# Kernel tuning notes

Measured on AMD Instinct MI355X. Metric: run time of the kernel, lower is better.

## Reference

```python
import jax, jax.numpy as jnp
import numpy as np

B, V, T = 64, 196, 64       # batch, visual tokens, text tokens
VIS, TXT, E = 768, 768, 512  # backbone dims, joint embed dim


def l2norm(x):
    return x / jnp.maximum(jnp.linalg.norm(x, axis=-1, keepdims=True), 1e-12)


def setup_inputs() -> dict:
    key = jax.random.key(0)
    ks = jax.random.split(key, 16)
    f = lambda k, s: jax.random.normal(k, s, dtype=jnp.float32)
    return {
        'v_cls': f(ks[0], (B, VIS)),
        'v_tok': f(ks[1], (B, V, VIS)),
        't_cls': f(ks[2], (B, TXT)),
        't_tok': f(ks[3], (B, T, TXT)),
        'Wv_cls': f(ks[4], (VIS, E)) * 0.02, 'bv_cls': jnp.zeros((E,), jnp.float32),
        'Wt_cls': f(ks[5], (TXT, E)) * 0.02, 'bt_cls': jnp.zeros((E,), jnp.float32),
        'Wv_tok': f(ks[6], (VIS, E)) * 0.02, 'bv_tok': jnp.zeros((E,), jnp.float32),
        'Wt_tok': f(ks[7], (TXT, E)) * 0.02, 'bt_tok': jnp.zeros((E,), jnp.float32),
        'wv_fc': f(ks[8], (E,)) * 0.02, 'bv_fc': jnp.zeros((), jnp.float32),
        'wt_fc': f(ks[9], (E,)) * 0.02, 'bt_fc': jnp.zeros((), jnp.float32),
        'text_length': jax.random.randint(ks[10], (B,), 16, T + 1),
    }


def reference(v_cls, v_tok, t_cls, t_tok,
              Wv_cls, bv_cls, Wt_cls, bt_cls,
              Wv_tok, bv_tok, Wt_tok, bt_tok,
              wv_fc, bv_fc, wt_fc, bt_fc, text_length):
    ve_cls = v_cls @ Wv_cls + bv_cls
    te_cls = t_cls @ Wt_cls + bt_cls
    ve = v_tok @ Wv_tok + bv_tok          # [B, V, E]
    te = t_tok @ Wt_tok + bt_tok          # [B, T, E]

    # per-token scalar weights (Linear(E, 1).squeeze(2))
    vw = ve @ wv_fc + bv_fc               # [B, V]
    tw = te @ wt_fc + bt_fc               # [B, T]

    # mask padded text positions (pos >= length), then softmax
    pad = jnp.arange(T)[None, :] >= text_length[:, None]
    tw = jax.nn.softmax(jnp.where(pad, -jnp.inf, tw), axis=-1)
    vw = jax.nn.softmax(vw, axis=-1)

    ve = l2norm(ve)
    te = l2norm(te)

    # full cross-batch token similarity [b, q, v, t]
    sim = jnp.einsum('bvd,qtd->bqvt', ve, te)
    image_to_text = jnp.einsum('bqv,bv->bq', sim.max(axis=-1), vw)
    text_to_image = jnp.einsum('bqt,qt->bq', sim.max(axis=2), tw)

    # diagonal (b == q) similarities drive the cdcr gathers
    sim_diag = jnp.einsum('bvd,btd->bvt', ve, te)
    idx1 = jnp.argmax(sim_diag, axis=-1)   # [B, V] best text token per visual token
    idx2 = jnp.argmax(sim_diag, axis=1)    # [B, T] best visual token per text token
    max_v = jnp.take_along_axis(ve, idx2[:, :, None], axis=1).reshape(-1, E)  # [B*T, E]
    max_t = jnp.take_along_axis(te, idx1[:, :, None], axis=1).reshape(-1, E)  # [B*V, E]

    t_feat = te.reshape(-1, E)
    v_feat = ve.reshape(-1, E)

    def zn(x):  # torch .std() is unbiased (ddof=1)
        return (x - x.mean(axis=0)) / jnp.std(x, axis=0, ddof=1)

    c1 = jnp.einsum('ac,ad,a->cd', zn(t_feat), zn(max_v), tw.reshape(-1)) / B
    c2 = jnp.einsum('ac,ad,a->cd', zn(v_feat), zn(max_t), vw.reshape(-1)) / B
    c = (c1 + c2) / 2.0

    D = c.shape[0]
    on_diag = jnp.sum((jnp.diagonal(c) - 1.0) ** 2)
    off_diag = jnp.sum(c.reshape(-1)[1:].reshape(D - 1, D + 1)[:, :-1] ** 2)
    cdcr_loss = 0.1 * (on_diag * 1.0 + off_diag * 0.06)

    return image_to_text, text_to_image, cdcr_loss
```

## Files before the change

kernel.cpp:

```cpp
#include <hip/hip_runtime.h>
#include <cstddef>

#define EDIM 512
#define KDIM 768
#define NB 64
#define NV 196
#define NT 64
#define MROWS_V (NB * NV)
#define MROWS_T (NB * NT)

typedef __attribute__((ext_vector_type(8))) short bf16x8;
typedef __attribute__((ext_vector_type(4))) float f32x4;

static __device__ inline unsigned short f2bf(float f) {
  unsigned u = __float_as_uint(f);
  unsigned r = (u + 0x7fff + ((u >> 16) & 1)) >> 16;
  return (unsigned short)r;
}
static __device__ inline float bf2f(short s) {
  return __uint_as_float(((unsigned)(unsigned short)s) << 16);
}
static __device__ __forceinline__ int swz4(int r) { return (r + (r >> 2)) & 3; }

static __device__ __forceinline__ void gload16(const void* g, void* l) {
  __builtin_amdgcn_global_load_lds(
      (const __attribute__((address_space(1))) void*)g,
      (__attribute__((address_space(3))) void*)l, 16, 0, 0);
}

__global__ void k_prep(const float* __restrict__ va, short* __restrict__ vo, int na8,
                       const float* __restrict__ ta, short* __restrict__ to, int nb8,
                       const float* __restrict__ W0, const float* __restrict__ W1,
                       short* __restrict__ T0, short* __restrict__ T1) {
  __shared__ float tile[32][33];
  int blk = blockIdx.x;
  int tid = threadIdx.x;
  if (blk < 6240) {
    int i = blk * 256 + tid;
    const float* in; short* outp; int idx;
    if (i < na8) { in = va; outp = vo; idx = i; }
    else { idx = i - na8; if (idx >= nb8) return; in = ta; outp = to; }
    float4 a = *(const float4*)(in + (size_t)idx * 8);
    float4 b = *(const float4*)(in + (size_t)idx * 8 + 4);
    bf16x8 v;
    v[0] = (short)f2bf(a.x); v[1] = (short)f2bf(a.y);
    v[2] = (short)f2bf(a.z); v[3] = (short)f2bf(a.w);
    v[4] = (short)f2bf(b.x); v[5] = (short)f2bf(b.y);
    v[6] = (short)f2bf(b.z); v[7] = (short)f2bf(b.w);
    *(bf16x8*)(outp + (size_t)idx * 8) = v;
  } else {
    int z = blk - 6240;
    int bx = z % 24, by = (z / 24) % 16, bz = z / 384;
    const float* W = bz ? W1 : W0;
    short*       T = bz ? T1 : T0;
    int k0 = bx * 32, n0 = by * 32;
    int tx = tid & 31, ty = tid >> 5;
    for (int i = ty; i < 32; i += 8)
      tile[i][tx] = W[(size_t)(k0 + i) * EDIM + n0 + tx];
    __syncthreads();
    for (int i = ty; i < 32; i += 8)
      T[(size_t)(n0 + i) * KDIM + k0 + tx] = (short)f2bf(tile[tx][i]);
  }
}

__global__ __launch_bounds__(256, 4) void k_proj_mfma2(
    const short* __restrict__ vX, const short* __restrict__ tX,
    const short* __restrict__ WvT, const short* __restrict__ WtT,
    const float* __restrict__ vb, const float* __restrict__ tb,
    short* __restrict__ vout, short* __restrict__ tout) {
  __shared__ short As[2][128 * 32];
  __shared__ short Bs[2][128 * 32];
  int y = blockIdx.y;
  const short* Xbf; const short* WT; const float* bias; short* Mbf; int r0;
  if (y < 98) { Xbf = vX; WT = WvT; bias = vb; Mbf = vout; r0 = y * 128; }
  else        { Xbf = tX; WT = WtT; bias = tb; Mbf = tout; r0 = (y - 98) * 128; }
  int n0 = blockIdx.x * 128;
  int tid = threadIdx.x;
  int w = tid >> 6, lane = tid & 63, lg = lane >> 4, li = lane & 15;
  int fsw = (li + (li >> 2)) & 3;

  const short* aSrc[2];
  const short* bSrc[2];
#pragma unroll
  for (int uu = 0; uu < 2; ++uu) {
    int u = uu * 256 + w * 64 + lane;
    int row = u >> 2, seg = u & 3;
    int ss = seg ^ swz4(row);
    aSrc[uu] = Xbf + (size_t)(r0 + row) * KDIM + ss * 8;
    bSrc[uu] = WT + (size_t)(n0 + row) * KDIM + ss * 8;
  }

  auto stage = [&](int bb) {
    short* Ad = &As[bb][0];
    short* Bd = &Bs[bb][0];
#pragma unroll
    for (int uu = 0; uu < 2; ++uu) {
      gload16(aSrc[uu], Ad + (uu * 256 + w * 64) * 8);
      aSrc[uu] += 32;
      gload16(bSrc[uu], Bd + (uu * 256 + w * 64) * 8);
      bSrc[uu] += 32;
    }
  };

  f32x4 acc[2][8];
#pragma unroll
  for (int i = 0; i < 2; ++i)
#pragma unroll
    for (int j = 0; j < 8; ++j) acc[i][j] = (f32x4){0.f, 0.f, 0.f, 0.f};

  stage(0);
  int cur = 0;
  const int NKC = KDIM / 32;
  for (int kc = 0; kc < NKC; ++kc) {
    __builtin_amdgcn_s_barrier();
    if (kc < NKC - 1) {
      stage(cur ^ 1);
      asm volatile("s_waitcnt vmcnt(4)" ::: "memory");
    } else {
      asm volatile("s_waitcnt vmcnt(0)" ::: "memory");
    }
    __builtin_amdgcn_s_barrier();
    const short* Ab = &As[cur][0];
    const short* Bb = &Bs[cur][0];
    bf16x8 bfr[8];
#pragma unroll
    for (int j = 0; j < 8; ++j)
      bfr[j] = *(const bf16x8*)(Bb + (j * 16 + li) * 32 + (lg ^ fsw) * 8);
    __builtin_amdgcn_s_setprio(1);
#pragma unroll
    for (int i = 0; i < 2; ++i) {
      bf16x8 afr = *(const bf16x8*)(Ab + ((w * 2 + i) * 16 + li) * 32 + (lg ^ fsw) * 8);
#pragma unroll
      for (int j = 0; j < 8; ++j)
        acc[i][j] = __builtin_amdgcn_mfma_f32_16x16x32_bf16(afr, bfr[j], acc[i][j], 0, 0, 0);
    }
    __builtin_amdgcn_s_setprio(0);
    cur ^= 1;
  }
#pragma unroll
  for (int j = 0; j < 8; ++j) {
    int n = n0 + j * 16 + li;
    float bb = bias[n];
#pragma unroll
    for (int i = 0; i < 2; ++i)
#pragma unroll
      for (int reg = 0; reg < 4; ++reg)
        Mbf[(size_t)(r0 + (w * 2 + i) * 16 + lg * 4 + reg) * EDIM + n] =
            (short)f2bf(acc[i][j][reg] + bb);
  }
}

__global__ void k_normfc2(short* __restrict__ vM, short* __restrict__ tM,
                          const float* __restrict__ vfcw, const float* __restrict__ tfcw,
                          const float* __restrict__ vfcb, const float* __restrict__ tfcb,
                          float* __restrict__ vwout, float* __restrict__ twout) {
  int blk = blockIdx.x;
  short* Mbf; const float* fcw; const float* fcb; float* wout; int row;
  if (blk < 3136) { Mbf = vM; fcw = vfcw; fcb = vfcb; wout = vwout;
                    row = blk * 4 + (threadIdx.x >> 6); if (row >= 12544) return; }
  else            { Mbf = tM; fcw = tfcw; fcb = tfcb; wout = twout;
                    row = (blk - 3136) * 4 + (threadIdx.x >> 6); if (row >= 4096) return; }
  int lane = threadIdx.x & 63;
  short* p = Mbf + (size_t)row * EDIM + lane * 8;
  bf16x8 v = *(bf16x8*)p;
  float4 w0 = *(const float4*)(fcw + lane * 8);
  float4 w1 = *(const float4*)(fcw + lane * 8 + 4);
  float a[8];
#pragma unroll
  for (int j = 0; j < 8; ++j) a[j] = bf2f(v[j]);
  float dot = a[0] * w0.x + a[1] * w0.y + a[2] * w0.z + a[3] * w0.w +
              a[4] * w1.x + a[5] * w1.y + a[6] * w1.z + a[7] * w1.w;
  float ss = a[0] * a[0] + a[1] * a[1] + a[2] * a[2] + a[3] * a[3] +
             a[4] * a[4] + a[5] * a[5] + a[6] * a[6] + a[7] * a[7];
  for (int s = 1; s < 64; s <<= 1) {
    dot += __shfl_xor(dot, s);
    ss += __shfl_xor(ss, s);
  }
  float inv = 1.0f / fmaxf(sqrtf(ss), 1e-12f);
#pragma unroll
  for (int j = 0; j < 8; ++j) v[j] = (short)f2bf(a[j] * inv);
  *(bf16x8*)p = v;
  if (lane == 0) wout[row] = dot + fcb[0];
}

__global__ void k_softmax(float* __restrict__ vwf, float* __restrict__ twf,
                          const int* __restrict__ tlen) {
  __shared__ float red[8];
  int tid = threadIdx.x;
  if (blockIdx.x < 64) {
    int b = blockIdx.x;
    float x = (tid < NV) ? vwf[b * NV + tid] : -1e30f;
    float m = x;
    for (int s = 1; s < 64; s <<= 1) m = fmaxf(m, __shfl_xor(m, s));
    if ((tid & 63) == 0) red[tid >> 6] = m;
    __syncthreads();
    m = fmaxf(fmaxf(red[0], red[1]), fmaxf(red[2], red[3]));
    float e = (tid < NV) ? expf(x - m) : 0.0f;
    float s = e;
    for (int st = 1; st < 64; st <<= 1) s += __shfl_xor(s, st);
    if ((tid & 63) == 0) red[4 + (tid >> 6)] = s;
    __syncthreads();
    s = red[4] + red[5] + red[6] + red[7];
    if (tid < NV) vwf[b * NV + tid] = e / s;
  } else {
    int b = blockIdx.x - 64;
    if (tid < 64) {
      int len = tlen[b];
      float x = twf[b * NT + tid];
      bool valid = tid < len;
      float xv = valid ? x : -1e30f;
      float m = xv;
      for (int s = 1; s < 64; s <<= 1) m = fmaxf(m, __shfl_xor(m, s));
      float e = valid ? expf(x - m) : 0.0f;
      float s = e;
      for (int st = 1; st < 64; st <<= 1) s += __shfl_xor(s, st);
      twf[b * NT + tid] = e / s;
    }
  }
}

__global__ __launch_bounds__(512, 4) void k_sim(
    const short* __restrict__ ve_bf, const short* __restrict__ te_bf,
    const float* __restrict__ vwf, const float* __restrict__ twf,
    float* __restrict__ out, int* __restrict__ gMT, int* __restrict__ gMV) {
  __shared__ short As[2][208 * 32];
  __shared__ short Bs[2][128 * 32];
  __shared__ float colv[8][64];
  __shared__ int   coli[8][64];
  __shared__ float redp[8];
  int n = blockIdx.x;
  int xcd = n & 7, idx = n >> 3;
  int b = xcd * 8 + (idx & 7);
  int qq = idx >> 3;
  int tid = threadIdx.x;
  int w = tid >> 6, lane = tid & 63, lg = lane >> 4, li = lane & 15;
  int qsel = w >> 2, wr = w & 3;
  int q = 2 * qq + qsel;
  const short* Abf = ve_bf + (size_t)b * NV * EDIM;
  const short* Bbf = te_bf + (size_t)qq * 128 * EDIM;
  int fsw = (li + (li >> 2)) & 3;
  int nt = wr ? 3 : 4;
  int tbase = wr ? (1 + wr * 3) : 0;

  const short* aSrc[2];
#pragma unroll
  for (int uu = 0; uu < 2; ++uu) {
    int u = uu * 512 + w * 64 + lane;
    int row = u >> 2;
    if (row > NV - 1) row = NV - 1;
    int seg = u & 3;
    int ss = seg ^ swz4(row);
    aSrc[uu] = Abf + (size_t)row * EDIM + ss * 8;
  }
  const short* bSrc;
  {
    int u = tid;
    int row = u >> 2, seg = u & 3;
    int ss = seg ^ swz4(row);
    bSrc = Bbf + (size_t)row * EDIM + ss * 8;
  }

  auto stage = [&](int bb) {
    short* Ad = &As[bb][0];
    short* Bd = &Bs[bb][0];
    gload16(bSrc, Bd + (w * 64) * 8);
    bSrc += 32;
#pragma unroll
    for (int uu = 0; uu < 2; ++uu) {
      int u0 = uu * 512 + w * 64;
      if (u0 < NV * 4) {
        gload16(aSrc[uu], Ad + u0 * 8);
        aSrc[uu] += 32;
      }
    }
  };

  f32x4 acc[4][4];
#pragma unroll
  for (int i = 0; i < 4; ++i)
#pragma unroll
    for (int j = 0; j < 4; ++j) acc[i][j] = (f32x4){0.f, 0.f, 0.f, 0.f};

  stage(0);
  int cur = 0;
  for (int kc = 0; kc < 16; ++kc) {
    __builtin_amdgcn_s_barrier();
    if (kc < 15) {
      stage(cur ^ 1);
      if (w <= 4) asm volatile("s_waitcnt vmcnt(3)" ::: "memory");
      else        asm volatile("s_waitcnt vmcnt(2)" ::: "memory");
    } else {
      asm volatile("s_waitcnt vmcnt(0)" ::: "memory");
    }
    __builtin_amdgcn_s_barrier();
    const short* Ab2 = &As[cur][0];
    const short* Bb2 = &Bs[cur][0];
    bf16x8 bfr[4];
#pragma unroll
    for (int j = 0; j < 4; ++j)
      bfr[j] = *(const bf16x8*)(Bb2 + (qsel * 64 + j * 16 + li) * 32 + (lg ^ fsw) * 8);
    __builtin_amdgcn_s_setprio(1);
#pragma unroll
    for (int i = 0; i < 4; ++i) {
      if (i < nt) {
        bf16x8 afr = *(const bf16x8*)(Ab2 + ((tbase + i) * 16 + li) * 32 + (lg ^ fsw) * 8);
#pragma unroll
        for (int j = 0; j < 4; ++j)
          acc[i][j] = __builtin_amdgcn_mfma_f32_16x16x32_bf16(afr, bfr[j], acc[i][j], 0, 0, 0);
      }
    }
    __builtin_amdgcn_s_setprio(0);
    cur ^= 1;
  }

  bool diag = (b == q);
  bool diagblk = (b >> 1) == qq;
  float ip = 0.f;

  if (diagblk) {
#pragma unroll
    for (int i = 0; i < 4; ++i) {
      if (i < nt) {
#pragma unroll
        for (int reg = 0; reg < 4; ++reg) {
          int v = (tbase + i) * 16 + lg * 4 + reg;
          float m = acc[i][0][reg];
          int ti = li;
#pragma unroll
          for (int j = 1; j < 4; ++j) {
            float vv = acc[i][j][reg];
            int t = j * 16 + li;
            if (vv > m) { m = vv; ti = t; }
          }
          for (int d = 1; d < 16; d <<= 1) {
            float om = __shfl_xor(m, d);
            int oi = __shfl_xor(ti, d);
            if (om > m || (om == m && oi < ti)) { m = om; ti = oi; }
          }
          if (li == 0 && v < NV) {
            ip += vwf[b * NV + v] * m;
            if (diag) gMT[b * NV + v] = b * NT + ti;
          }
        }
      }
    }
    float cm[4]; int cv[4];
#pragma unroll
    for (int j = 0; j < 4; ++j) { cm[j] = -3.0e38f; cv[j] = 0; }
#pragma unroll
    for (int i = 0; i < 4; ++i) {
      if (i < nt) {
#pragma unroll
        for (int reg = 0; reg < 4; ++reg) {
          int v = (tbase + i) * 16 + lg * 4 + reg;
          bool ok = v < NV;
#pragma unroll
          for (int j = 0; j < 4; ++j) {
            float s = ok ? acc[i][j][reg] : -3.0e38f;
            if (s > cm[j]) { cm[j] = s; cv[j] = v; }
          }
        }
      }
    }
#pragma unroll
    for (int j = 0; j < 4; ++j) {
      for (int d = 16; d < 64; d <<= 1) {
        float om = __shfl_xor(cm[j], d);
        int ov = __shfl_xor(cv[j], d);
        if (om > cm[j] || (om == cm[j] && ov < cv[j])) { cm[j] = om; cv[j] = ov; }
      }
      if (lg == 0) { colv[w][j * 16 + li] = cm[j]; coli[w][j * 16 + li] = cv[j]; }
    }
  } else {
#pragma unroll
    for (int i = 0; i < 4; ++i) {
      if (i < nt) {
#pragma unroll
        for (int reg = 0; reg < 4; ++reg) {
          int v = (tbase + i) * 16 + lg * 4 + reg;
          float m = fmaxf(fmaxf(acc[i][0][reg], acc[i][1][reg]),
                          fmaxf(acc[i][2][reg], acc[i][3][reg]));
          for (int d = 1; d < 16; d <<= 1) m = fmaxf(m, __shfl_xor(m, d));
          if (li == 0 && v < NV) ip += vwf[b * NV + v] * m;
        }
      }
    }
    float cm[4];
#pragma unroll
    for (int j = 0; j < 4; ++j) cm[j] = -3.0e38f;
#pragma unroll
    for (int i = 0; i < 4; ++i) {
      if (i < nt) {
#pragma unroll
      for (int reg = 0; reg < 4; ++reg) {
          int v = (tbase + i) * 16 + lg * 4 + reg;
          bool ok = v < NV;
#pragma unroll
          for (int j = 0; j < 4; ++j)
            cm[j] = fmaxf(cm[j], ok ? acc[i][j][reg] : -3.0e38f);
        }
      }
    }
#pragma unroll
    for (int j = 0; j < 4; ++j) {
      for (int d = 16; d < 64; d <<= 1) cm[j] = fmaxf(cm[j], __shfl_xor(cm[j], d));
      if (lg == 0) colv[w][j * 16 + li] = cm[j];
    }
  }
  for (int d = 1; d < 64; d <<= 1) ip += __shfl_xor(ip, d);
  if (lane == 0) redp[w] = ip;
  __syncthreads();
  if (tid < 128) {
    int qs = tid >> 6, t = tid & 63;
    int qe = 2 * qq + qs;
    float m = colv[qs * 4][t];
    if (diagblk) {
      int bi = coli[qs * 4][t];
#pragma unroll
      for (int w2 = 1; w2 < 4; ++w2) {
        float om = colv[qs * 4 + w2][t];
        int ov = coli[qs * 4 + w2][t];
        if (om > m || (om == m && ov < bi)) { m = om; bi = ov; }
      }
      if (b == qe) gMV[b * NT + t] = b * NV + bi;
    } else {
#pragma unroll
      for (int w2 = 1; w2 < 4; ++w2) m = fmaxf(m, colv[qs * 4 + w2][t]);
    }
    float p = twf[qe * NT + t] * m;
    for (int d = 1; d < 64; d <<= 1) p += __shfl_xor(p, d);
    if ((tid & 63) == 0) out[4096 + b * 64 + qe] = p;
  }
  if (tid == 0) {
    out[b * 64 + 2 * qq]     = redp[0] + redp[1] + redp[2] + redp[3];
    out[b * 64 + 2 * qq + 1] = redp[4] + redp[5] + redp[6] + redp[7];
  }
}

__global__ void k_materialize(const short* __restrict__ ve_bf, const short* __restrict__ te_bf,
                              const int* __restrict__ gMT, const int* __restrict__ gMV,
                              const float* __restrict__ vwf, const float* __restrict__ twf,
                              short* __restrict__ tTw, short* __restrict__ mvT,
                              short* __restrict__ vTw, short* __restrict__ mtT,
                              float* __restrict__ statPart) {
  int z = blockIdx.z;
  int at = blockIdx.x, ct = blockIdx.y;
  int K = (z == 2 || z == 3) ? MROWS_V : MROWS_T;
  if (at * 64 >= K) return;
  const short* src; const int* g = 0; short* dst;
  bool applyW;
  const float* wS = (z <= 1) ? twf : vwf;
  if (z == 0)      { src = te_bf; dst = tTw; applyW = true;  }
  else if (z == 1) { src = ve_bf; g = gMV; dst = mvT; applyW = false; }
  else if (z == 2) { src = ve_bf; dst = vTw; applyW = true;  }
  else             { src = te_bf; g = gMT; dst = mtT; applyW = false; }
  __shared__ float tile[64][67];
  __shared__ float wrow[64];
  int tid = threadIdx.x;
  for (int u = tid; u < 512; u += 256) {
    int a = u >> 3, cseg = (u & 7) << 3;
    int ga = at * 64 + a;
    int row = g ? g[ga] : ga;
    bf16x8 vv = *(const bf16x8*)(src + (size_t)row * EDIM + ct * 64 + cseg);
#pragma unroll
    for (int j = 0; j < 8; j++) tile[a][cseg + j] = bf2f(vv[j]);
    if ((u & 7) == 0) wrow[a] = wS[ga];
  }
  __syncthreads();
  for (int u = tid; u < 512; u += 256) {
    int c = u >> 3, aseg = (u & 7) << 3;
    bf16x8 ov;
#pragma unroll
    for (int j = 0; j < 8; j++) {
      float x = tile[aseg + j][c];
      if (applyW) x *= wrow[aseg + j];
      ov[j] = (short)f2bf(x);
    }
    int kchunk = at * 2 + (aseg >> 5);
    *(bf16x8*)(dst + ((size_t)kchunk * 512 + ct * 64 + c) * 32 + (aseg & 31)) = ov;
  }
  int cl = tid >> 2, part = tid & 3;
  float s = 0, ssq = 0, sw = 0;
  for (int a = part * 16; a < part * 16 + 16; ++a) {
    float x = tile[a][cl];
    s += x; ssq += x * x; sw += wrow[a] * x;
  }
  for (int d = 1; d < 4; d <<= 1) {
    s += __shfl_xor(s, d); ssq += __shfl_xor(ssq, d); sw += __shfl_xor(sw, d);
  }
  if (part == 0) {
    int cbase = (z == 0) ? 0 : (z == 1) ? 64 : (z == 2) ? 128 : 324;
    size_t sidx = ((size_t)(cbase + at) * 512 + ct * 64 + cl) * 3;
    statPart[sidx] = s; statPart[sidx + 1] = ssq; statPart[sidx + 2] = sw;
  }
}

__global__ void k_statfin(const float* __restrict__ statPart, float* __restrict__ stats) {
  int m = blockIdx.x, c = threadIdx.x;
  int R = (m < 2) ? MROWS_T : MROWS_V;
  int nchunk = (m < 2) ? 64 : 196;
  int base = (m == 0) ? 0 : (m == 1) ? 64 : (m == 2) ? 128 : 324;
  float s = 0, ss = 0, sw = 0;
  for (int ch = 0; ch < nchunk; ch++) {
    size_t idx = ((size_t)(base + ch) * 512 + c) * 3;
    s += statPart[idx]; ss += statPart[idx + 1]; sw += statPart[idx + 2];
  }
  float mean = s / R;
  float var = (ss - s * mean) / (R - 1);
  float rstd = 1.0f / sqrtf(var);
  stats[(m * 3 + 0) * 512 + c] = mean;
  stats[(m * 3 + 1) * 512 + c] = rstd;
  stats[(m * 3 + 2) * 512 + c] = sw;
}

__global__ __launch_bounds__(512, 2) void k_wgemm2(
    const short* __restrict__ tTw, const short* __restrict__ mvT,
    const short* __restrict__ vTw, const short* __restrict__ mtT,
    float* __restrict__ Spart) {
  __shared__ short As[2][128 * 32];
  __shared__ short Bs[2][128 * 32];
  int c0 = blockIdx.x * 128, d0 = blockIdx.y * 128;
  int z = blockIdx.z;
  int which = z >> 3, slice = z & 7;
  const short* A = which ? vTw : tTw;
  const short* B = which ? mtT : mvT;
  int K = which ? MROWS_V : MROWS_T;
  int nch = (K >> 3) >> 5;
  size_t a0c = (size_t)slice * nch;
  int tid = threadIdx.x;
  int w = tid >> 6, lane = tid & 63, lg = lane >> 4, li = lane & 15;
  int fsw = (li + (li >> 2)) & 3;

  const short* aSrc; const short* bSrc;
  {
    int row = tid >> 2, seg = tid & 3;
    int ss = seg ^ swz4(row);
    aSrc = A + (a0c * 512 + (size_t)(c0 + row)) * 32 + ss * 8;
    bSrc = B + (a0c * 512 + (size_t)(d0 + row)) * 32 + ss * 8;
  }

  auto stage = [&](int bb) {
    gload16(aSrc, &As[bb][0] + (w * 64) * 8);
    aSrc += 512 * 32;
    gload16(bSrc, &Bs[bb][0] + (w * 64) * 8);
    bSrc += 512 * 32;
  };

  f32x4 acc[8];
#pragma unroll
  for (int j = 0; j < 8; ++j) acc[j] = (f32x4){0.f, 0.f, 0.f, 0.f};

  stage(0);
  int cur = 0;
  for (int ch = 0; ch < nch; ++ch) {
    __builtin_amdgcn_s_barrier();
    if (ch < nch - 1) {
      stage(cur ^ 1);
      asm volatile("s_waitcnt vmcnt(2)" ::: "memory");
    } else {
      asm volatile("s_waitcnt vmcnt(0)" ::: "memory");
    }
    __builtin_amdgcn_s_barrier();
    const short* Ab = &As[cur][0];
    const short* Bb = &Bs[cur][0];
    bf16x8 afr = *(const bf16x8*)(Ab + (w * 16 + li) * 32 + (lg ^ fsw) * 8);
    __builtin_amdgcn_s_setprio(1);
#pragma unroll
    for (int j = 0; j < 8; ++j) {
      bf16x8 bfr = *(const bf16x8*)(Bb + (j * 16 + li) * 32 + (lg ^ fsw) * 8);
      acc[j] = __builtin_amdgcn_mfma_f32_16x16x32_bf16(afr, bfr, acc[j], 0, 0, 0);
    }
    __builtin_amdgcn_s_setprio(0);
    cur ^= 1;
  }
  float* outp = Spart + (size_t)z * 512 * 512;
#pragma unroll
  for (int j = 0; j < 8; ++j) {
    int d = d0 + j * 16 + li;
#pragma unroll
    for (int reg = 0; reg < 4; ++reg)
      outp[(size_t)(c0 + w * 16 + lg * 4 + reg) * 512 + d] = acc[j][reg];
  }
}

__global__ void k_assemble(const float* __restrict__ Spart, const float* __restrict__ stats,
                           float* __restrict__ lossPart) {
  int c = blockIdx.x, tid = threadIdx.x;
  float muT = stats[0 * 512 + c], rsT = stats[1 * 512 + c], swT = stats[2 * 512 + c];
  float muV = stats[6 * 512 + c], rsV = stats[7 * 512 + c], swV = stats[8 * 512 + c];
  const float W = 64.0f, invB = 1.0f / 64.0f;
  float on = 0, off = 0;
  for (int d = tid; d < 512; d += 256) {
    float s1 = 0, s2 = 0;
    for (int sl = 0; sl < 8; sl++) {
      s1 += Spart[((size_t)sl * 512 + c) * 512 + d];
      s2 += Spart[((size_t)(8 + sl) * 512 + c) * 512 + d];
    }
    float muMV = stats[3 * 512 + d], rsMV = stats[4 * 512 + d], swMV = stats[5 * 512 + d];
    float muMT = stats[9 * 512 + d], rsMT = stats[10 * 512 + d], swMT = stats[11 * 512 + d];
    float c1 = (s1 - muT * swMV - muMV * swT + muT * muMV * W) * rsT * rsMV * invB;
    float c2 = (s2 - muV * swMT - muMT * swV + muV * muMT * W) * rsV * rsMT * invB;
    float cc = 0.5f * (c1 + c2);
    if (d == c) { float dd = cc - 1.0f; on += dd * dd; }
    else off += cc * cc;
  }
  __shared__ float r1[4], r2[4];
  for (int s = 1; s < 64; s <<= 1) { on += __shfl_xor(on, s); off += __shfl_xor(off, s); }
  if ((tid & 63) == 0) { r1[tid >> 6] = on; r2[tid >> 6] = off; }
  __syncthreads();
  if (tid == 0) {
    lossPart[c * 2] = r1[0] + r1[1] + r1[2] + r1[3];
    lossPart[c * 2 + 1] = r2[0] + r2[1] + r2[2] + r2[3];
  }
}

__global__ void k_loss(const float* __restrict__ lossPart, float* __restrict__ out) {
  int tid = threadIdx.x;
  float on = 0, off = 0;
  for (int i = tid; i < 512; i += 256) { on += lossPart[2 * i]; off += lossPart[2 * i + 1]; }
  __shared__ float r1[4], r2[4];
  for (int s = 1; s < 64; s <<= 1) { on += __shfl_xor(on, s); off += __shfl_xor(off, s); }
  if ((tid & 63) == 0) { r1[tid >> 6] = on; r2[tid >> 6] = off; }
  __syncthreads();
  if (tid == 0)
    out[8192] = 0.1f * ((r1[0] + r1[1] + r1[2] + r1[3]) +
                        0.06f * (r2[0] + r2[1] + r2[2] + r2[3]));
}

extern "C" void kernel_launch(void* const* d_in, const int* in_sizes, int n_in,
                              void* d_out, int out_size, void* d_ws, size_t ws_size,
                              hipStream_t stream) {
  (void)in_sizes; (void)n_in; (void)out_size; (void)ws_size;
  const float* v_tok  = (const float*)d_in[1];
  const float* t_tok  = (const float*)d_in[3];
  const float* Wv_tok = (const float*)d_in[8];
  const float* Wt_tok = (const float*)d_in[10];
  const float* bv_tok = (const float*)d_in[9];
  const float* bt_tok = (const float*)d_in[11];
  const float* wv_fc  = (const float*)d_in[12];
  const float* bv_fc  = (const float*)d_in[13];
  const float* wt_fc  = (const float*)d_in[14];
  const float* bt_fc  = (const float*)d_in[15];
  const int*   tlen   = (const int*)d_in[16];
  float* out = (float*)d_out;

  char* wsb = (char*)d_ws;
  short* v_tok_bf = (short*)wsb;
  short* t_tok_bf = v_tok_bf + (size_t)9633792;
  short* WvT      = t_tok_bf + (size_t)3145728;
  short* WtT      = WvT + (size_t)393216;
  short* tTw = (short*)wsb;
  short* mvT = tTw + (size_t)2097152;
  short* vTw = mvT + (size_t)2097152;
  short* ve_bf = (short*)(wsb + 27131904);
  short* te_bf = ve_bf + (size_t)6422528;
  float* Spart = (float*)(wsb + 27131904);
  short* mtT = (short*)(wsb + 44171264);
  float* vwf = (float*)(wsb + 57016320);
  float* twf = vwf + 12544;
  int* gMT = (int*)(twf + 4096);
  int* gMV = gMT + 12544;
  float* statPart = (float*)(gMV + 4096);
  float* stats = statPart + (size_t)520 * 512 * 3;
  float* lossPart = stats + 6144;

  k_prep<<<7008, 256, 0, stream>>>(v_tok, v_tok_bf, 1204224, t_tok, t_tok_bf, 393216,
                                   Wv_tok, Wt_tok, WvT, WtT);
  k_proj_mfma2<<<dim3(4, 130), 256, 0, stream>>>(v_tok_bf, t_tok_bf, WvT, WtT,
                                                 bv_tok, bt_tok, ve_bf, te_bf);
  k_normfc2<<<4160, 256, 0, stream>>>(ve_bf, te_bf, wv_fc, wt_fc, bv_fc, bt_fc, vwf, twf);
  k_softmax<<<128, 256, 0, stream>>>(vwf, twf, tlen);
  k_sim<<<2048, 512, 0, stream>>>(ve_bf, te_bf, vwf, twf, out, gMT, gMV);
  k_materialize<<<dim3(196, 8, 4), 256, 0, stream>>>(ve_bf, te_bf, gMT, gMV, vwf, twf,
                                                     tTw, mvT, vTw, mtT, statPart);
  k_statfin<<<4, 512, 0, stream>>>(statPart, stats);
  k_wgemm2<<<dim3(4, 4, 16), 512, 0, stream>>>(tTw, mvT, vTw, mtT, Spart);
  k_assemble<<<512, 256, 0, stream>>>(Spart, stats, lossPart);
  k_loss<<<1, 256, 0, stream>>>(lossPart, out);
}
```

Baseline: 247.0 us.

## Fold stat finalization into weighted GEMM launch and rebalance K-slices

Removes the separate k_statfin launch by handling the four stat-finalization blocks as an extra z-slice of k_wgemm2. Also rebalances the split-K work: the shorter text GEMM now gets 4 slices and the longer visual GEMM gets 12 slices of about 32-33 chunks each, rather than 8 slices for each. This saves one launch and evens out per-block work. The cost is that k_assemble now reads 12 visual partials instead of 8, and some wgemm blocks exit early.

```diff
diff --git a/kernel.cpp b/kernel.cpp
--- a/kernel.cpp
+++ b/kernel.cpp
@@ -495,38 +495,44 @@
   }
 }
 
-__global__ void k_statfin(const float* __restrict__ statPart, float* __restrict__ stats) {
-  int m = blockIdx.x, c = threadIdx.x;
-  int R = (m < 2) ? MROWS_T : MROWS_V;
-  int nchunk = (m < 2) ? 64 : 196;
-  int base = (m == 0) ? 0 : (m == 1) ? 64 : (m == 2) ? 128 : 324;
-  float s = 0, ss = 0, sw = 0;
-  for (int ch = 0; ch < nchunk; ch++) {
-    size_t idx = ((size_t)(base + ch) * 512 + c) * 3;
-    s += statPart[idx]; ss += statPart[idx + 1]; sw += statPart[idx + 2];
-  }
-  float mean = s / R;
-  float var = (ss - s * mean) / (R - 1);
-  float rstd = 1.0f / sqrtf(var);
-  stats[(m * 3 + 0) * 512 + c] = mean;
-  stats[(m * 3 + 1) * 512 + c] = rstd;
-  stats[(m * 3 + 2) * 512 + c] = sw;
-}
-
 __global__ __launch_bounds__(512, 2) void k_wgemm2(
     const short* __restrict__ tTw, const short* __restrict__ mvT,
     const short* __restrict__ vTw, const short* __restrict__ mtT,
+    const float* __restrict__ statPart, float* __restrict__ stats,
     float* __restrict__ Spart) {
+  int z = blockIdx.z;
+  if (z == 16) {
+    if (blockIdx.y != 0 || blockIdx.x >= 4) return;
+    int m = blockIdx.x;
+    int R = (m < 2) ? MROWS_T : MROWS_V;
+    int nchunk = (m < 2) ? 64 : 196;
+    int base = (m == 0) ? 0 : (m == 1) ? 64 : (m == 2) ? 128 : 324;
+    int c = threadIdx.x;
+    float s = 0, ss = 0, sw = 0;
+    for (int ch = 0; ch < nchunk; ch++) {
+      size_t idx = ((size_t)(base + ch) * 512 + c) * 3;
+      s += statPart[idx]; ss += statPart[idx + 1]; sw += statPart[idx + 2];
+    }
+    float mean = s / R;
+    float var = (ss - s * mean) / (R - 1);
+    float rstd = 1.0f / sqrtf(var);
+    stats[(m * 3 + 0) * 512 + c] = mean;
+    stats[(m * 3 + 1) * 512 + c] = rstd;
+    stats[(m * 3 + 2) * 512 + c] = sw;
+    return;
+  }
   __shared__ short As[2][128 * 32];
   __shared__ short Bs[2][128 * 32];
   int c0 = blockIdx.x * 128, d0 = blockIdx.y * 128;
-  int z = blockIdx.z;
-  int which = z >> 3, slice = z & 7;
-  const short* A = which ? vTw : tTw;
-  const short* B = which ? mtT : mvT;
-  int K = which ? MROWS_V : MROWS_T;
-  int nch = (K >> 3) >> 5;
-  size_t a0c = (size_t)slice * nch;
+  const short* A; const short* B; int nch; size_t a0c;
+  if (z < 4) {
+    A = tTw; B = mvT; nch = 32; a0c = (size_t)z * 32;
+  } else {
+    A = vTw; B = mtT;
+    int vi = z - 4;
+    if (vi < 8) { nch = 33; a0c = (size_t)vi * 33; }
+    else        { nch = 32; a0c = 264 + (size_t)(vi - 8) * 32; }
+  }
   int tid = threadIdx.x;
   int w = tid >> 6, lane = tid & 63, lg = lane >> 4, li = lane & 15;
   int fsw = (li + (li >> 2)) & 3;
@@ -592,10 +598,12 @@
   float on = 0, off = 0;
   for (int d = tid; d < 512; d += 256) {
     float s1 = 0, s2 = 0;
-    for (int sl = 0; sl < 8; sl++) {
+#pragma unroll
+    for (int sl = 0; sl < 4; sl++)
       s1 += Spart[((size_t)sl * 512 + c) * 512 + d];
-      s2 += Spart[((size_t)(8 + sl) * 512 + c) * 512 + d];
-    }
+#pragma unroll
+    for (int sl = 4; sl < 16; sl++)
+      s2 += Spart[((size_t)sl * 512 + c) * 512 + d];
     float muMV = stats[3 * 512 + d], rsMV = stats[4 * 512 + d], swMV = stats[5 * 512 + d];
     float muMT = stats[9 * 512 + d], rsMT = stats[10 * 512 + d], swMT = stats[11 * 512 + d];
     float c1 = (s1 - muT * swMV - muMV * swT + muT * muMV * W) * rsT * rsMV * invB;
@@ -673,8 +681,7 @@
   k_sim<<<2048, 512, 0, stream>>>(ve_bf, te_bf, vwf, twf, out, gMT, gMV);
   k_materialize<<<dim3(196, 8, 4), 256, 0, stream>>>(ve_bf, te_bf, gMT, gMV, vwf, twf,
                                                      tTw, mvT, vTw, mtT, statPart);
-  k_statfin<<<4, 512, 0, stream>>>(statPart, stats);
-  k_wgemm2<<<dim3(4, 4, 16), 512, 0, stream>>>(tTw, mvT, vTw, mtT, Spart);
+  k_wgemm2<<<dim3(4, 4, 17), 512, 0, stream>>>(tTw, mvT, vTw, mtT, statPart, stats, Spart);
   k_assemble<<<512, 256, 0, stream>>>(Spart, stats, lossPart);
   k_loss<<<1, 256, 0, stream>>>(lossPart, out);
 }
```

After: 218.5 us. 11.5% less time.
